# Kernel tuning notes

Measured on AMD Instinct MI355X. Metric: run time of the kernel, lower is better.

## Reference

```python
import jax, jax.numpy as jnp
import numpy as np
from jax import lax

B = 128

# ---- 4-qubit statevector helpers (RY + CNOT circuit is real-valued) ----

def _init_state(n):
    s = jnp.zeros((n, 2, 2, 2, 2), jnp.float32)
    return s.at[:, 0, 0, 0, 0].set(1.0)


def _ry(state, theta, wire):
    # RY(t) = [[cos t/2, -sin t/2],[sin t/2, cos t/2]]; theta: scalar or [N]
    s = jnp.moveaxis(state, wire + 1, 1)
    c = jnp.cos(theta * 0.5)
    sn = jnp.sin(theta * 0.5)
    if jnp.ndim(theta) > 0:
        c = c.reshape(-1, 1, 1, 1)
        sn = sn.reshape(-1, 1, 1, 1)
    a, b = s[:, 0], s[:, 1]
    s = jnp.stack([c * a - sn * b, sn * a + c * b], axis=1)
    return jnp.moveaxis(s, 1, wire + 1)


def _cnot(state, ctrl, tgt):
    s = jnp.moveaxis(state, [ctrl + 1, tgt + 1], [1, 2])
    s = jnp.concatenate([s[:, :1], jnp.flip(s[:, 1:], axis=2)], axis=1)
    return jnp.moveaxis(s, [1, 2], [ctrl + 1, tgt + 1])


def _random_layer(state, thetas):
    for i in range(4):
        state = _ry(state, thetas[i], i)
        state = _cnot(state, i, (i + 1) % 4)
    return state


def _measure_z(state, wire):
    p = jnp.moveaxis(state, wire + 1, 1) ** 2
    p = p.reshape(p.shape[0], 2, -1).sum(-1)
    return p[:, 0] - p[:, 1]


def setup_inputs() -> dict:
    key = jax.random.key(0)
    ks = jax.random.split(key, 12)

    def n(k, shape, scale):
        return jax.random.normal(k, shape, jnp.float32) * scale

    return {
        "x": jax.random.normal(ks[0], (B, 3, 249, 249), jnp.float32),
        "conv1_w": n(ks[1], (6, 3, 5, 5), 0.1),
        "conv1_b": jnp.zeros((6,), jnp.float32),
        "conv2_w": n(ks[2], (15, 6, 3, 3), 0.1),
        "conv2_b": jnp.zeros((15,), jnp.float32),
        "fc1_w": n(ks[3], (120, 55815), 1.0 / np.sqrt(55815.0)),
        "fc1_b": jnp.zeros((120,), jnp.float32),
        "fc2_w": n(ks[4], (84, 120), 1.0 / np.sqrt(120.0)),
        "fc2_b": jnp.zeros((84,), jnp.float32),
        "fc3_w": n(ks[5], (1, 84), 1.0 / np.sqrt(84.0)),
        "fc3_b": jnp.zeros((1,), jnp.float32),
        "head_thetas": jax.random.uniform(ks[6], (4,), jnp.float32, 0.0, 2.0 * np.pi),
        "qf_thetas": jax.random.uniform(ks[7], (4,), jnp.float32, 0.0, 2.0 * np.pi),
        "lin_w": n(ks[8], (1, 784), 1.0 / np.sqrt(784.0)),
        "lin_b": jnp.zeros((1,), jnp.float32),
    }


def reference(x, conv1_w, conv1_b, conv2_w, conv2_b, fc1_w, fc1_b, fc2_w, fc2_b,
              fc3_w, fc3_b, head_thetas, qf_thetas, lin_w, lin_b):
    bsz = x.shape[0]

    def conv(y, w, b, stride):
        y = lax.conv_general_dilated(y, w, (stride, stride), [(1, 1), (1, 1)],
                                     dimension_numbers=("NCHW", "OIHW", "NCHW"))
        return y + b[None, :, None, None]

    def pool(y):  # MaxPool2d(kernel=2, stride=1)
        return lax.reduce_window(y, -jnp.inf, lax.max, (1, 1, 2, 2), (1, 1, 1, 1), "VALID")

    # ---- conv branch (dropout = identity in eval) ----
    h = pool(jax.nn.relu(conv(x, conv1_w, conv1_b, 2)))          # [B,6,123,123]
    h = pool(jax.nn.relu(conv(h, conv2_w, conv2_b, 2)))          # [B,15,61,61]
    h = h.reshape(bsz, -1)                                        # [B,55815]
    h = jax.nn.relu(h @ fc1_w.T + fc1_b)
    h = jax.nn.relu(h @ fc2_w.T + fc2_b)
    logit = (h @ fc3_w.T + fc3_b)[:, 0]                           # [B]
    st = _init_state(bsz)
    st = _ry(st, logit, 0)
    st = _random_layer(st, head_thetas)
    probs_conv = jax.nn.sigmoid(_measure_z(st, 0))[:, None]       # [B,1]

    # ---- quanvolution branch ----
    gray = x.mean(axis=1, keepdims=True)                          # [B,1,249,249]
    g = jax.image.resize(gray, (bsz, 1, 28, 28), method="linear")[:, 0]
    # 2x2 patches, row-major, element order [tl, tr, bl, br]
    patches = g.reshape(bsz, 14, 2, 14, 2).transpose(0, 1, 3, 2, 4).reshape(bsz * 196, 4)
    st = _init_state(bsz * 196)
    for w in range(4):
        st = _ry(st, patches[:, w], w)
    st = _random_layer(st, qf_thetas)
    feats = jnp.stack([_measure_z(st, w) for w in range(4)], axis=1).reshape(bsz, 784)
    probs_q = jax.nn.sigmoid(feats @ lin_w.T + lin_b)             # [B,1]

    probs = (probs_conv + probs_q) * 0.5
    return jnp.concatenate([probs, 1.0 - probs], axis=-1)         # [B,2]
```

## Files before the change

kernel.cpp:

```cpp
#include <hip/hip_runtime.h>
#include <math.h>

#define DEV static __device__ __forceinline__

template <int W>
DEV void q_ry(float s[16], float th) {
  float c = cosf(th * 0.5f), sn = sinf(th * 0.5f);
  constexpr int m = 8 >> W;
#pragma unroll
  for (int i = 0; i < 16; ++i) {
    if (!(i & m)) {
      float a = s[i], b = s[i | m];
      s[i] = c * a - sn * b;
      s[i | m] = sn * a + c * b;
    }
  }
}
template <int C, int T>
DEV void q_cnot(float s[16]) {
  constexpr int mc = 8 >> C, mt = 8 >> T;
#pragma unroll
  for (int i = 0; i < 16; ++i) {
    if ((i & mc) && !(i & mt)) {
      float t = s[i]; s[i] = s[i | mt]; s[i | mt] = t;
    }
  }
}
template <int W>
DEV float q_mz(const float s[16]) {
  constexpr int m = 8 >> W;
  float p = 0.f;
#pragma unroll
  for (int i = 0; i < 16; ++i) p += (i & m) ? -s[i] * s[i] : s[i] * s[i];
  return p;
}
DEV void q_layer(float s[16], const float* __restrict__ th) {
  q_ry<0>(s, th[0]); q_cnot<0, 1>(s);
  q_ry<1>(s, th[1]); q_cnot<1, 2>(s);
  q_ry<2>(s, th[2]); q_cnot<2, 3>(s);
  q_ry<3>(s, th[3]); q_cnot<3, 0>(s);
}

__global__ __launch_bounds__(256, 4) void k_conv1(const float* __restrict__ x,
                                                  const float* __restrict__ w,
                                                  const float* __restrict__ bia,
                                                  float* __restrict__ out) {
  __shared__ float smem[3 * 87 * 38];
  float (*xs)[87][38] = (float (*)[87][38])smem;
  float (*ct)[42][19] = (float (*)[42][19])smem;
  int b = blockIdx.z;
  int PY0 = blockIdx.y * 41, PX0 = blockIdx.x * 16;
  int iy0 = PY0 * 2 - 1, ix0 = PX0 * 2 - 1;
  int tid = threadIdx.x;
  const float* xb = x + (size_t)b * 186003;
  for (int idx = tid; idx < 3 * 87 * 38; idx += 256) {
    int ci = idx / 3306, rem = idx % 3306, rr = rem / 38, cc = rem % 38;
    int iy = iy0 + rr, ix = ix0 + cc;
    float v = 0.f;
    if (cc < 37 && iy >= 0 && iy < 249 && ix >= 0 && ix < 249)
      v = xb[ci * 62001 + iy * 249 + ix];
    xs[ci][rr][cc] = v;
  }
  __syncthreads();
  int co = tid % 6, r = tid / 6;
  float acc[17];
  if (tid < 252) {
    float bv = bia[co];
#pragma unroll
    for (int t = 0; t < 17; ++t) acc[t] = bv;
    for (int ci = 0; ci < 3; ++ci) {
      float wreg[25];
#pragma unroll
      for (int j = 0; j < 25; ++j) wreg[j] = w[co * 75 + ci * 25 + j];
#pragma unroll
      for (int ky = 0; ky < 5; ++ky) {
        const float* xrow = &xs[ci][2 * r + ky][0];
        float xv[38];
#pragma unroll
        for (int j = 0; j < 19; ++j) {
          float2 t2 = *reinterpret_cast<const float2*>(&xrow[2 * j]);
          xv[2 * j] = t2.x; xv[2 * j + 1] = t2.y;
        }
#pragma unroll
        for (int tx = 0; tx < 17; ++tx)
#pragma unroll
          for (int kx = 0; kx < 5; ++kx)
            acc[tx] += xv[2 * tx + kx] * wreg[ky * 5 + kx];
      }
    }
  }
  __syncthreads();
  if (tid < 252) {
#pragma unroll
    for (int tx = 0; tx < 17; ++tx) ct[co][r][tx] = acc[tx];
  }
  __syncthreads();
  for (int i = tid; i < 6 * 41 * 16; i += 256) {
    int co2 = i / 656, rem = i % 656, pr = rem / 16, pc = rem % 16;
    int py = PY0 + pr, px = PX0 + pc;
    if (px < 123) {
      float m = fmaxf(fmaxf(ct[co2][pr][pc], ct[co2][pr][pc + 1]),
                      fmaxf(ct[co2][pr + 1][pc], ct[co2][pr + 1][pc + 1]));
      out[((size_t)(b * 6 + co2) * 123 + py) * 123 + px] = fmaxf(m, 0.f);
    }
  }
}

__global__ __launch_bounds__(256, 4) void k_conv2(const float* __restrict__ in,
                                                  const float* __restrict__ w,
                                                  const float* __restrict__ bia,
                                                  float* __restrict__ out) {
  __shared__ float smem[6 * 35 * 36];
  float (*xs)[35][36] = (float (*)[35][36])smem;
  float (*ct)[17][18] = (float (*)[17][18])smem;
  int b = blockIdx.z;
  int py0 = blockIdx.y * 16, px0 = blockIdx.x * 16;
  int iy0 = py0 * 2 - 1, ix0 = px0 * 2 - 1;
  int tid = threadIdx.x;
  const float* ib = in + (size_t)b * 90774;
  for (int idx = tid; idx < 6 * 35 * 36; idx += 256) {
    int ci = idx / 1260, rem = idx % 1260, rr = rem / 36, cc = rem % 36;
    int iy = iy0 + rr, ix = ix0 + cc;
    float v = 0.f;
    if (cc < 35 && iy >= 0 && iy < 123 && ix >= 0 && ix < 123)
      v = ib[ci * 15129 + iy * 123 + ix];
    xs[ci][rr][cc] = v;
  }
  __syncthreads();
  int co = tid % 15, ty = tid / 15;
  float acc[17];
  if (tid < 255) {
    float bv = bia[co];
#pragma unroll
    for (int t = 0; t < 17; ++t) acc[t] = bv;
#pragma unroll
    for (int ci = 0; ci < 6; ++ci) {
      float wreg[9];
#pragma unroll
      for (int j = 0; j < 9; ++j) wreg[j] = w[co * 54 + ci * 9 + j];
#pragma unroll
      for (int ky = 0; ky < 3; ++ky) {
        const float* xrow = &xs[ci][2 * ty + ky][0];
        float xv[36];
#pragma unroll
        for (int j = 0; j < 18; ++j) {
          float2 t2 = *reinterpret_cast<const float2*>(&xrow[2 * j]);
          xv[2 * j] = t2.x; xv[2 * j + 1] = t2.y;
        }
#pragma unroll
        for (int tx = 0; tx < 17; ++tx)
#pragma unroll
          for (int kx = 0; kx < 3; ++kx)
            acc[tx] += xv[2 * tx + kx] * wreg[ky * 3 + kx];
      }
    }
  }
  __syncthreads();
  if (tid < 255) {
#pragma unroll
    for (int tx = 0; tx < 17; ++tx) ct[co][ty][tx] = acc[tx];
  }
  __syncthreads();
  for (int i = tid; i < 15 * 16 * 16; i += 256) {
    int co2 = i / 256, rem = i % 256, pr = rem / 16, pc = rem % 16;
    int py = py0 + pr, px = px0 + pc;
    if (py < 61 && px < 61) {
      float m = fmaxf(fmaxf(ct[co2][pr][pc], ct[co2][pr][pc + 1]),
                      fmaxf(ct[co2][pr + 1][pc], ct[co2][pr + 1][pc + 1]));
      out[(size_t)b * 55815 + co2 * 3721 + py * 61 + px] = fmaxf(m, 0.f);
    }
  }
}

#define KFC 55815
#define NCHUNK 1745
#define FC1_BLOCKS 512
__global__ __launch_bounds__(256) void k_fc1(const float* __restrict__ h,
                                             const float* __restrict__ w,
                                             float* __restrict__ partial) {
  __shared__ float hs[128][33];
  __shared__ float wsd[120][33];
  int tid = threadIdx.x;
  int tb = tid & 31;
  int bo = tid >> 5;
  float acc[4][15];
#pragma unroll
  for (int j = 0; j < 4; ++j)
#pragma unroll
    for (int oo = 0; oo < 15; ++oo) acc[j][oo] = 0.f;

  for (int ch = blockIdx.x; ch < NCHUNK; ch += FC1_BLOCKS) {
    int k0 = ch * 32;
    for (int idx = tid; idx < 128 * 32; idx += 256) {
      int bb = idx >> 5, kk = idx & 31;
      int k = k0 + kk;
      hs[bb][kk] = (k < KFC) ? h[(size_t)bb * KFC + k] : 0.f;
    }
    for (int idx = tid; idx < 120 * 32; idx += 256) {
      int oo = idx >> 5, kk = idx & 31;
      int k = k0 + kk;
      wsd[oo][kk] = (k < KFC) ? w[(size_t)oo * KFC + k] : 0.f;
    }
    __syncthreads();
#pragma unroll 4
    for (int kk = 0; kk < 32; ++kk) {
      float hv[4], wv[15];
#pragma unroll
      for (int j = 0; j < 4; ++j) hv[j] = hs[tb + 32 * j][kk];
#pragma unroll
      for (int oo = 0; oo < 15; ++oo) wv[oo] = wsd[bo * 15 + oo][kk];
#pragma unroll
      for (int j = 0; j < 4; ++j)
#pragma unroll
        for (int oo = 0; oo < 15; ++oo) acc[j][oo] += hv[j] * wv[oo];
    }
    __syncthreads();
  }
  float* pg = partial + (size_t)blockIdx.x * 15360;
#pragma unroll
  for (int j = 0; j < 4; ++j) {
    int b = tb + 32 * j;
#pragma unroll
    for (int oo = 0; oo < 15; ++oo) pg[b * 120 + bo * 15 + oo] = acc[j][oo];
  }
}

__global__ __launch_bounds__(256) void k_fc1_reduce(const float* __restrict__ partial,
                                                    const float* __restrict__ bias,
                                                    float* __restrict__ outv) {
  int i = blockIdx.x * 256 + threadIdx.x;
  if (i >= 15360) return;
  float a = bias[i % 120];
  for (int g = 0; g < FC1_BLOCKS; ++g) a += partial[(size_t)g * 15360 + i];
  outv[i] = fmaxf(a, 0.f);
}

__global__ __launch_bounds__(128) void k_head(const float* __restrict__ fc1o,
                                              const float* __restrict__ w2,
                                              const float* __restrict__ b2,
                                              const float* __restrict__ w3,
                                              const float* __restrict__ b3,
                                              const float* __restrict__ hth,
                                              float* __restrict__ probs_conv) {
  __shared__ float h1[120];
  __shared__ float h2[84];
  int b = blockIdx.x, tid = threadIdx.x;
  if (tid < 120) h1[tid] = fc1o[b * 120 + tid];
  __syncthreads();
  if (tid < 84) {
    float a = b2[tid];
    for (int k = 0; k < 120; ++k) a += h1[k] * w2[tid * 120 + k];
    h2[tid] = fmaxf(a, 0.f);
  }
  __syncthreads();
  if (tid == 0) {
    float lg = b3[0];
    for (int j = 0; j < 84; ++j) lg += h2[j] * w3[j];
    float s[16];
#pragma unroll
    for (int i = 0; i < 16; ++i) s[i] = 0.f;
    s[0] = 1.f;
    q_ry<0>(s, lg);
    q_layer(s, hth);
    float z = q_mz<0>(s);
    probs_conv[b] = 1.f / (1.f + expf(-z));
  }
}

DEV void resize_win(int o, int& i0, int& i1, float& sf, float& inorm) {
  const float invs = 249.0f / 28.0f;
  sf = ((float)o + 0.5f) * invs - 0.5f;
  i0 = (int)ceilf(sf - invs); if (i0 < 0) i0 = 0;
  i1 = (int)floorf(sf + invs); if (i1 > 248) i1 = 248;
  float nrm = 0.f;
  for (int i = i0; i <= i1; ++i)
    nrm += fmaxf(0.f, 1.f - fabsf(sf - (float)i) * (28.0f / 249.0f));
  inorm = 1.f / nrm;
}

__global__ __launch_bounds__(256) void k_resize_rows(const float* __restrict__ x,
                                                     float* __restrict__ tmp) {
  int b = blockIdx.x / 28, oy = blockIdx.x % 28;
  int ix = threadIdx.x;
  if (ix >= 249) return;
  int i0, i1; float sf, inorm;
  resize_win(oy, i0, i1, sf, inorm);
  const float* xb = x + (size_t)b * 186003;
  float acc = 0.f;
  for (int iy = i0; iy <= i1; ++iy) {
    float wv = fmaxf(0.f, 1.f - fabsf(sf - (float)iy) * (28.0f / 249.0f)) * inorm;
    float gr = (xb[iy * 249 + ix] + xb[62001 + iy * 249 + ix] +
                xb[124002 + iy * 249 + ix]) * (1.0f / 3.0f);
    acc += wv * gr;
  }
  tmp[((size_t)b * 28 + oy) * 249 + ix] = acc;
}

__global__ __launch_bounds__(256) void k_quanv(const float* __restrict__ tmp,
                                               const float* __restrict__ qth,
                                               const float* __restrict__ lw,
                                               const float* __restrict__ lb,
                                               const float* __restrict__ probs_conv,
                                               float* __restrict__ out) {
  __shared__ float g[784];
  __shared__ float red[4];
  int b = blockIdx.x, tid = threadIdx.x;
  for (int idx = tid; idx < 784; idx += 256) {
    int oy = idx / 28, ox = idx % 28;
    int i0, i1; float sf, inorm;
    resize_win(ox, i0, i1, sf, inorm);
    const float* tr = tmp + ((size_t)b * 28 + oy) * 249;
    float acc = 0.f;
    for (int i = i0; i <= i1; ++i)
      acc += fmaxf(0.f, 1.f - fabsf(sf - (float)i) * (28.0f / 249.0f)) * inorm * tr[i];
    g[idx] = acc;
  }
  __syncthreads();
  float part = 0.f;
  if (tid < 196) {
    int pi = tid / 14, pj = tid % 14;
    float v0 = g[(2 * pi) * 28 + 2 * pj];
    float v1 = g[(2 * pi) * 28 + 2 * pj + 1];
    float v2 = g[(2 * pi + 1) * 28 + 2 * pj];
    float v3 = g[(2 * pi + 1) * 28 + 2 * pj + 1];
    float s[16];
#pragma unroll
    for (int i = 0; i < 16; ++i) s[i] = 0.f;
    s[0] = 1.f;
    q_ry<0>(s, v0); q_ry<1>(s, v1); q_ry<2>(s, v2); q_ry<3>(s, v3);
    q_layer(s, qth);
    float z0 = q_mz<0>(s), z1 = q_mz<1>(s), z2 = q_mz<2>(s), z3 = q_mz<3>(s);
    const float* lwp = lw + tid * 4;
    part = z0 * lwp[0] + z1 * lwp[1] + z2 * lwp[2] + z3 * lwp[3];
  }
#pragma unroll
  for (int off = 32; off > 0; off >>= 1) part += __shfl_down(part, off, 64);
  if ((tid & 63) == 0) red[tid >> 6] = part;
  __syncthreads();
  if (tid == 0) {
    float tot = red[0] + red[1] + red[2] + red[3] + lb[0];
    float pq = 1.f / (1.f + expf(-tot));
    float pr = 0.5f * (probs_conv[b] + pq);
    out[b * 2 + 0] = pr;
    out[b * 2 + 1] = 1.f - pr;
  }
}

extern "C" void kernel_launch(void* const* d_in, const int* in_sizes, int n_in,
                              void* d_out, int out_size, void* d_ws, size_t ws_size,
                              hipStream_t stream) {
  const float* x   = (const float*)d_in[0];
  const float* c1w = (const float*)d_in[1];
  const float* c1b = (const float*)d_in[2];
  const float* c2w = (const float*)d_in[3];
  const float* c2b = (const float*)d_in[4];
  const float* f1w = (const float*)d_in[5];
  const float* f1b = (const float*)d_in[6];
  const float* f2w = (const float*)d_in[7];
  const float* f2b = (const float*)d_in[8];
  const float* f3w = (const float*)d_in[9];
  const float* f3b = (const float*)d_in[10];
  const float* hth = (const float*)d_in[11];
  const float* qth = (const float*)d_in[12];
  const float* lw  = (const float*)d_in[13];
  const float* lb  = (const float*)d_in[14];
  float* out = (float*)d_out;
  char* ws = (char*)d_ws;

  float* pool1   = (float*)(ws);
  float* partial = pool1;
  float* h       = (float*)(ws + 46476288);
  float* tmp     = (float*)(ws + 75053568);
  float* fc1o    = (float*)(ws + 78623232);
  float* pconv   = (float*)(ws + 78684672);

  k_conv1<<<dim3(8, 3, 128), 256, 0, stream>>>(x, c1w, c1b, pool1);
  k_conv2<<<dim3(4, 4, 128), 256, 0, stream>>>(pool1, c2w, c2b, h);
  k_fc1<<<dim3(FC1_BLOCKS), 256, 0, stream>>>(h, f1w, partial);
  k_fc1_reduce<<<dim3(60), 256, 0, stream>>>(partial, f1b, fc1o);
  k_head<<<dim3(128), 128, 0, stream>>>(fc1o, f2w, f2b, f3w, f3b, hth, pconv);
  k_resize_rows<<<dim3(128 * 28), 256, 0, stream>>>(x, tmp);
  k_quanv<<<dim3(128), 256, 0, stream>>>(tmp, qth, lw, lb, pconv, out);
}
```

Baseline: 283.0 us.

## Restructure conv1/conv2 so each thread computes all output channels over column segments

The conv kernels change their thread mapping. Before, each thread handled one output channel across a full row of 17 columns. Now each thread computes every output channel for a small column segment, so each loaded input value is reused across channels. A new small pre-kernel reorders the conv weights so each (ci,ky) slice loads as a contiguous block. conv2 also uses taller tiles (31 rows) and stages input channels in two phases to fit shared memory, which halves the block count in y. The risks are extra register pressure from the larger accumulator and weight arrays, uneven work for the thread that handles the last column in conv2, and one extra kernel launch.

```diff
diff --git a/kernel.cpp b/kernel.cpp
--- a/kernel.cpp
+++ b/kernel.cpp
@@ -41,133 +41,190 @@
   q_ry<3>(s, th[3]); q_cnot<3, 0>(s);
 }
 
+__global__ void k_wre(const float* __restrict__ c1w, const float* __restrict__ c2w,
+                      float* __restrict__ wre1, float* __restrict__ wre2) {
+  int t = blockIdx.x * 256 + threadIdx.x;
+  if (t < 450) {
+    int g = t / 30, rem = t % 30;
+    int ci = g / 5, ky = g % 5, kx = rem / 6, co = rem % 6;
+    wre1[t] = c1w[co * 75 + ci * 25 + ky * 5 + kx];
+  }
+  if (t < 810) {
+    int g = t / 45, rem = t % 45;
+    int ci = g / 3, ky = g % 3, kx = rem / 15, co = rem % 15;
+    wre2[t] = c2w[co * 54 + ci * 9 + ky * 3 + kx];
+  }
+}
+
 __global__ __launch_bounds__(256, 4) void k_conv1(const float* __restrict__ x,
-                                                  const float* __restrict__ w,
+                                                  const float* __restrict__ wre1,
                                                   const float* __restrict__ bia,
                                                   float* __restrict__ out) {
-  __shared__ float smem[3 * 87 * 38];
-  float (*xs)[87][38] = (float (*)[87][38])smem;
+  __shared__ float smem[9920];
   float (*ct)[42][19] = (float (*)[42][19])smem;
   int b = blockIdx.z;
   int PY0 = blockIdx.y * 41, PX0 = blockIdx.x * 16;
   int iy0 = PY0 * 2 - 1, ix0 = PX0 * 2 - 1;
   int tid = threadIdx.x;
   const float* xb = x + (size_t)b * 186003;
-  for (int idx = tid; idx < 3 * 87 * 38; idx += 256) {
-    int ci = idx / 3306, rem = idx % 3306, rr = rem / 38, cc = rem % 38;
+#pragma unroll
+  for (int s = 0; s < 39; ++s) {
+    int idx = s * 256 + tid;
+    bool ok = idx < 9918;
+    int ci = idx / 3306, rem = idx - ci * 3306;
+    int rr = rem / 38, cc = rem - rr * 38;
     int iy = iy0 + rr, ix = ix0 + cc;
     float v = 0.f;
-    if (cc < 37 && iy >= 0 && iy < 249 && ix >= 0 && ix < 249)
+    if (ok && cc < 37 && (unsigned)iy < 249u && (unsigned)ix < 249u)
       v = xb[ci * 62001 + iy * 249 + ix];
-    xs[ci][rr][cc] = v;
-  }
-  __syncthreads();
-  int co = tid % 6, r = tid / 6;
-  float acc[17];
+    if (ok) smem[idx] = v;
+  }
+  __syncthreads();
+  int r = tid / 6, seg = tid - 6 * (tid / 6);
+  float acc[6][3];
   if (tid < 252) {
-    float bv = bia[co];
-#pragma unroll
-    for (int t = 0; t < 17; ++t) acc[t] = bv;
-    for (int ci = 0; ci < 3; ++ci) {
-      float wreg[25];
-#pragma unroll
-      for (int j = 0; j < 25; ++j) wreg[j] = w[co * 75 + ci * 25 + j];
+#pragma unroll
+    for (int co = 0; co < 6; ++co) {
+      float bv = bia[co];
+#pragma unroll
+      for (int c = 0; c < 3; ++c) acc[co][c] = bv;
+    }
+#pragma unroll
+    for (int ci = 0; ci < 3; ++ci)
 #pragma unroll
       for (int ky = 0; ky < 5; ++ky) {
-        const float* xrow = &xs[ci][2 * r + ky][0];
-        float xv[38];
-#pragma unroll
-        for (int j = 0; j < 19; ++j) {
+        const float* xrow = &smem[(ci * 87 + 2 * r + ky) * 38 + 6 * seg];
+        float xv[10];
+#pragma unroll
+        for (int j = 0; j < 5; ++j) {
           float2 t2 = *reinterpret_cast<const float2*>(&xrow[2 * j]);
           xv[2 * j] = t2.x; xv[2 * j + 1] = t2.y;
         }
-#pragma unroll
-        for (int tx = 0; tx < 17; ++tx)
+        const float* wp = wre1 + (ci * 5 + ky) * 30;
+        float wr[30];
+#pragma unroll
+        for (int j = 0; j < 30; ++j) wr[j] = wp[j];
+#pragma unroll
+        for (int c = 0; c < 3; ++c)
 #pragma unroll
           for (int kx = 0; kx < 5; ++kx)
-            acc[tx] += xv[2 * tx + kx] * wreg[ky * 5 + kx];
+#pragma unroll
+            for (int co = 0; co < 6; ++co)
+              acc[co][c] += xv[2 * c + kx] * wr[kx * 6 + co];
       }
-    }
   }
   __syncthreads();
   if (tid < 252) {
 #pragma unroll
-    for (int tx = 0; tx < 17; ++tx) ct[co][r][tx] = acc[tx];
-  }
-  __syncthreads();
-  for (int i = tid; i < 6 * 41 * 16; i += 256) {
-    int co2 = i / 656, rem = i % 656, pr = rem / 16, pc = rem % 16;
-    int py = PY0 + pr, px = PX0 + pc;
-    if (px < 123) {
-      float m = fmaxf(fmaxf(ct[co2][pr][pc], ct[co2][pr][pc + 1]),
-                      fmaxf(ct[co2][pr + 1][pc], ct[co2][pr + 1][pc + 1]));
-      out[((size_t)(b * 6 + co2) * 123 + py) * 123 + px] = fmaxf(m, 0.f);
+    for (int co = 0; co < 6; ++co)
+#pragma unroll
+      for (int c = 0; c < 3; ++c)
+        if (3 * seg + c < 17) ct[co][r][3 * seg + c] = acc[co][c];
+  }
+  __syncthreads();
+#pragma unroll
+  for (int co2 = 0; co2 < 6; ++co2) {
+    for (int j = tid; j < 41 * 16; j += 256) {
+      int pr = j >> 4, pc = j & 15;
+      int px = PX0 + pc;
+      if (px < 123) {
+        float m = fmaxf(fmaxf(ct[co2][pr][pc], ct[co2][pr][pc + 1]),
+                        fmaxf(ct[co2][pr + 1][pc], ct[co2][pr + 1][pc + 1]));
+        out[((size_t)(b * 6 + co2) * 123 + PY0 + pr) * 123 + px] = fmaxf(m, 0.f);
+      }
     }
   }
 }
 
 __global__ __launch_bounds__(256, 4) void k_conv2(const float* __restrict__ in,
-                                                  const float* __restrict__ w,
+                                                  const float* __restrict__ wre2,
                                                   const float* __restrict__ bia,
                                                   float* __restrict__ out) {
-  __shared__ float smem[6 * 35 * 36];
-  float (*xs)[35][36] = (float (*)[35][36])smem;
-  float (*ct)[17][18] = (float (*)[17][18])smem;
+  __shared__ float smem[8160];
+  float (*ct)[32][17] = (float (*)[32][17])smem;
   int b = blockIdx.z;
-  int py0 = blockIdx.y * 16, px0 = blockIdx.x * 16;
-  int iy0 = py0 * 2 - 1, ix0 = px0 * 2 - 1;
+  int ty_tile = blockIdx.y;
+  int CY0 = ty_tile * 31;
+  int CX0 = blockIdx.x * 16;
+  int IY0 = 2 * CY0 - 1, IX0 = 2 * CX0 - 1;
   int tid = threadIdx.x;
+  int r = tid >> 3, seg = tid & 7;
   const float* ib = in + (size_t)b * 90774;
-  for (int idx = tid; idx < 6 * 35 * 36; idx += 256) {
-    int ci = idx / 1260, rem = idx % 1260, rr = rem / 36, cc = rem % 36;
-    int iy = iy0 + rr, ix = ix0 + cc;
-    float v = 0.f;
-    if (cc < 35 && iy >= 0 && iy < 123 && ix >= 0 && ix < 123)
-      v = ib[ci * 15129 + iy * 123 + ix];
-    xs[ci][rr][cc] = v;
-  }
-  __syncthreads();
-  int co = tid % 15, ty = tid / 15;
-  float acc[17];
-  if (tid < 255) {
+  float acc[15][3];
+#pragma unroll
+  for (int co = 0; co < 15; ++co) {
     float bv = bia[co];
 #pragma unroll
-    for (int t = 0; t < 17; ++t) acc[t] = bv;
-#pragma unroll
-    for (int ci = 0; ci < 6; ++ci) {
-      float wreg[9];
-#pragma unroll
-      for (int j = 0; j < 9; ++j) wreg[j] = w[co * 54 + ci * 9 + j];
+    for (int c = 0; c < 3; ++c) acc[co][c] = bv;
+  }
+#pragma unroll
+  for (int phase = 0; phase < 2; ++phase) {
+    if (phase) __syncthreads();
+#pragma unroll
+    for (int s = 0; s < 28; ++s) {
+      int idx = s * 256 + tid;
+      bool ok = idx < 7020;
+      int cil = idx / 2340, rem = idx - cil * 2340;
+      int rr = rem / 36, cc = rem - rr * 36;
+      int iy = IY0 + rr, ix = IX0 + cc;
+      float v = 0.f;
+      if (ok && cc < 35 && (unsigned)iy < 123u && (unsigned)ix < 123u)
+        v = ib[(3 * phase + cil) * 15129 + iy * 123 + ix];
+      if (ok) smem[idx] = v;
+    }
+    __syncthreads();
+#pragma unroll
+    for (int cil = 0; cil < 3; ++cil)
 #pragma unroll
       for (int ky = 0; ky < 3; ++ky) {
-        const float* xrow = &xs[ci][2 * ty + ky][0];
-        float xv[36];
-#pragma unroll
-        for (int j = 0; j < 18; ++j) {
+        const float* xrow = &smem[(cil * 65 + 2 * r + ky) * 36 + 4 * seg];
+        float xv[8];
+#pragma unroll
+        for (int j = 0; j < 4; ++j) {
           float2 t2 = *reinterpret_cast<const float2*>(&xrow[2 * j]);
           xv[2 * j] = t2.x; xv[2 * j + 1] = t2.y;
         }
-#pragma unroll
-        for (int tx = 0; tx < 17; ++tx)
+        const float* wp = wre2 + ((3 * phase + cil) * 3 + ky) * 45;
+        float wr[45];
+#pragma unroll
+        for (int j = 0; j < 45; ++j) wr[j] = wp[j];
+#pragma unroll
+        for (int c = 0; c < 2; ++c)
 #pragma unroll
           for (int kx = 0; kx < 3; ++kx)
-            acc[tx] += xv[2 * tx + kx] * wreg[ky * 3 + kx];
+#pragma unroll
+            for (int co = 0; co < 15; ++co)
+              acc[co][c] += xv[2 * c + kx] * wr[kx * 15 + co];
+        if (seg == 7) {
+#pragma unroll
+          for (int kx = 0; kx < 3; ++kx)
+#pragma unroll
+            for (int co = 0; co < 15; ++co)
+              acc[co][2] += xv[4 + kx] * wr[kx * 15 + co];
+        }
       }
-    }
-  }
-  __syncthreads();
-  if (tid < 255) {
-#pragma unroll
-    for (int tx = 0; tx < 17; ++tx) ct[co][ty][tx] = acc[tx];
-  }
-  __syncthreads();
-  for (int i = tid; i < 15 * 16 * 16; i += 256) {
-    int co2 = i / 256, rem = i % 256, pr = rem / 16, pc = rem % 16;
-    int py = py0 + pr, px = px0 + pc;
-    if (py < 61 && px < 61) {
-      float m = fmaxf(fmaxf(ct[co2][pr][pc], ct[co2][pr][pc + 1]),
-                      fmaxf(ct[co2][pr + 1][pc], ct[co2][pr + 1][pc + 1]));
-      out[(size_t)b * 55815 + co2 * 3721 + py * 61 + px] = fmaxf(m, 0.f);
+  }
+  __syncthreads();
+  if (CY0 + r < 62) {
+#pragma unroll
+    for (int co = 0; co < 15; ++co) {
+      ct[co][r][2 * seg] = acc[co][0];
+      ct[co][r][2 * seg + 1] = acc[co][1];
+      if (seg == 7) ct[co][r][16] = acc[co][2];
+    }
+  }
+  __syncthreads();
+  int PRN = (ty_tile == 0) ? 31 : 30;
+#pragma unroll
+  for (int co2 = 0; co2 < 15; ++co2) {
+    for (int j = tid; j < PRN * 16; j += 256) {
+      int pr = j >> 4, pc = j & 15;
+      int py = CY0 + pr, px = CX0 + pc;
+      if (px < 61) {
+        float m = fmaxf(fmaxf(ct[co2][pr][pc], ct[co2][pr][pc + 1]),
+                        fmaxf(ct[co2][pr + 1][pc], ct[co2][pr + 1][pc + 1]));
+        out[(size_t)b * 55815 + co2 * 3721 + py * 61 + px] = fmaxf(m, 0.f);
+      }
     }
   }
 }
@@ -373,9 +430,12 @@
   float* tmp     = (float*)(ws + 75053568);
   float* fc1o    = (float*)(ws + 78623232);
   float* pconv   = (float*)(ws + 78684672);
-
-  k_conv1<<<dim3(8, 3, 128), 256, 0, stream>>>(x, c1w, c1b, pool1);
-  k_conv2<<<dim3(4, 4, 128), 256, 0, stream>>>(pool1, c2w, c2b, h);
+  float* wre1    = (float*)(ws + 78685184);
+  float* wre2    = (float*)(ws + 78686984);
+
+  k_wre<<<dim3(4), 256, 0, stream>>>(c1w, c2w, wre1, wre2);
+  k_conv1<<<dim3(8, 3, 128), 256, 0, stream>>>(x, wre1, c1b, pool1);
+  k_conv2<<<dim3(4, 2, 128), 256, 0, stream>>>(pool1, wre2, c2b, h);
   k_fc1<<<dim3(FC1_BLOCKS), 256, 0, stream>>>(h, f1w, partial);
   k_fc1_reduce<<<dim3(60), 256, 0, stream>>>(partial, f1b, fc1o);
   k_head<<<dim3(128), 128, 0, stream>>>(fc1o, f2w, f2b, f3w, f3b, hth, pconv);
```

New measurement: 429.3 us. 1.52x slower.

## Restructure conv1 thread mapping to compute all output channels per thread segment

Applied to the files above, without the earlier changes.

conv1 now assigns each thread a row and a 3-column segment and accumulates all six output channels, with weights pre-transposed by a small k_wre kernel so each weight load feeds six channels and the per-thread input window shrinks. The smem staging loop is fully unrolled with unsigned bounds checks. The pool1 output row stride is padded to 128, and conv2 reads with the padded stride. The quanvolution kernel is split into two half-image blocks per batch item, with a tiny final kernel combining the partial sums, which adds two extra launches.

```diff
diff --git a/kernel.cpp b/kernel.cpp
--- a/kernel.cpp
+++ b/kernel.cpp
@@ -41,67 +41,88 @@
   q_ry<3>(s, th[3]); q_cnot<3, 0>(s);
 }
 
+__global__ void k_wre(const float* __restrict__ c1w, float* __restrict__ wre1) {
+  int t = blockIdx.x * 256 + threadIdx.x;
+  if (t < 450) {
+    int g = t / 30, rem = t % 30;
+    int ci = g / 5, ky = g % 5, kx = rem / 6, co = rem % 6;
+    wre1[t] = c1w[co * 75 + ci * 25 + ky * 5 + kx];
+  }
+}
+
 __global__ __launch_bounds__(256, 4) void k_conv1(const float* __restrict__ x,
-                                                  const float* __restrict__ w,
+                                                  const float* __restrict__ wre1,
                                                   const float* __restrict__ bia,
                                                   float* __restrict__ out) {
-  __shared__ float smem[3 * 87 * 38];
-  float (*xs)[87][38] = (float (*)[87][38])smem;
+  __shared__ float smem[9920];
   float (*ct)[42][19] = (float (*)[42][19])smem;
   int b = blockIdx.z;
   int PY0 = blockIdx.y * 41, PX0 = blockIdx.x * 16;
   int iy0 = PY0 * 2 - 1, ix0 = PX0 * 2 - 1;
   int tid = threadIdx.x;
   const float* xb = x + (size_t)b * 186003;
-  for (int idx = tid; idx < 3 * 87 * 38; idx += 256) {
-    int ci = idx / 3306, rem = idx % 3306, rr = rem / 38, cc = rem % 38;
+#pragma unroll
+  for (int s = 0; s < 39; ++s) {
+    int idx = s * 256 + tid;
+    bool ok = idx < 9918;
+    int ci = idx / 3306, rem = idx - ci * 3306;
+    int rr = rem / 38, cc = rem - rr * 38;
     int iy = iy0 + rr, ix = ix0 + cc;
     float v = 0.f;
-    if (cc < 37 && iy >= 0 && iy < 249 && ix >= 0 && ix < 249)
+    if (ok && cc < 37 && (unsigned)iy < 249u && (unsigned)ix < 249u)
       v = xb[ci * 62001 + iy * 249 + ix];
-    xs[ci][rr][cc] = v;
-  }
-  __syncthreads();
-  int co = tid % 6, r = tid / 6;
-  float acc[17];
+    if (ok) smem[idx] = v;
+  }
+  __syncthreads();
+  int r = tid / 6, seg = tid - 6 * (tid / 6);
+  float acc[6][3];
   if (tid < 252) {
-    float bv = bia[co];
-#pragma unroll
-    for (int t = 0; t < 17; ++t) acc[t] = bv;
-    for (int ci = 0; ci < 3; ++ci) {
-      float wreg[25];
-#pragma unroll
-      for (int j = 0; j < 25; ++j) wreg[j] = w[co * 75 + ci * 25 + j];
+#pragma unroll
+    for (int co = 0; co < 6; ++co) {
+      float bv = bia[co];
+#pragma unroll
+      for (int c = 0; c < 3; ++c) acc[co][c] = bv;
+    }
+#pragma unroll
+    for (int ci = 0; ci < 3; ++ci)
 #pragma unroll
       for (int ky = 0; ky < 5; ++ky) {
-        const float* xrow = &xs[ci][2 * r + ky][0];
-        float xv[38];
-#pragma unroll
-        for (int j = 0; j < 19; ++j) {
+        const float* xrow = &smem[(ci * 87 + 2 * r + ky) * 38 + 6 * seg];
+        float xv[10];
+#pragma unroll
+        for (int j = 0; j < 5; ++j) {
           float2 t2 = *reinterpret_cast<const float2*>(&xrow[2 * j]);
           xv[2 * j] = t2.x; xv[2 * j + 1] = t2.y;
         }
-#pragma unroll
-        for (int tx = 0; tx < 17; ++tx)
+        const float* wp = wre1 + (ci * 5 + ky) * 30;
+        float wr[30];
+#pragma unroll
+        for (int j = 0; j < 30; ++j) wr[j] = wp[j];
+#pragma unroll
+        for (int c = 0; c < 3; ++c)
 #pragma unroll
           for (int kx = 0; kx < 5; ++kx)
-            acc[tx] += xv[2 * tx + kx] * wreg[ky * 5 + kx];
+#pragma unroll
+            for (int co = 0; co < 6; ++co)
+              acc[co][c] += xv[2 * c + kx] * wr[kx * 6 + co];
       }
-    }
   }
   __syncthreads();
   if (tid < 252) {
 #pragma unroll
-    for (int tx = 0; tx < 17; ++tx) ct[co][r][tx] = acc[tx];
-  }
-  __syncthreads();
-  for (int i = tid; i < 6 * 41 * 16; i += 256) {
-    int co2 = i / 656, rem = i % 656, pr = rem / 16, pc = rem % 16;
-    int py = PY0 + pr, px = PX0 + pc;
-    if (px < 123) {
+    for (int co = 0; co < 6; ++co)
+#pragma unroll
+      for (int c = 0; c < 3; ++c)
+        if (3 * seg + c < 17) ct[co][r][3 * seg + c] = acc[co][c];
+  }
+  __syncthreads();
+#pragma unroll
+  for (int co2 = 0; co2 < 6; ++co2) {
+    for (int j = tid; j < 41 * 16; j += 256) {
+      int pr = j >> 4, pc = j & 15;
       float m = fmaxf(fmaxf(ct[co2][pr][pc], ct[co2][pr][pc + 1]),
                       fmaxf(ct[co2][pr + 1][pc], ct[co2][pr + 1][pc + 1]));
-      out[((size_t)(b * 6 + co2) * 123 + py) * 123 + px] = fmaxf(m, 0.f);
+      out[((size_t)(b * 6 + co2) * 123 + PY0 + pr) * 128 + PX0 + pc] = fmaxf(m, 0.f);
     }
   }
 }
@@ -117,13 +138,13 @@
   int py0 = blockIdx.y * 16, px0 = blockIdx.x * 16;
   int iy0 = py0 * 2 - 1, ix0 = px0 * 2 - 1;
   int tid = threadIdx.x;
-  const float* ib = in + (size_t)b * 90774;
+  const float* ib = in + (size_t)b * 94464;
   for (int idx = tid; idx < 6 * 35 * 36; idx += 256) {
     int ci = idx / 1260, rem = idx % 1260, rr = rem / 36, cc = rem % 36;
     int iy = iy0 + rr, ix = ix0 + cc;
     float v = 0.f;
-    if (cc < 35 && iy >= 0 && iy < 123 && ix >= 0 && ix < 123)
-      v = ib[ci * 15129 + iy * 123 + ix];
+    if (cc < 35 && (unsigned)iy < 123u && (unsigned)ix < 123u)
+      v = ib[ci * 15744 + iy * 128 + ix];
     xs[ci][rr][cc] = v;
   }
   __syncthreads();
@@ -299,14 +320,15 @@
 __global__ __launch_bounds__(256) void k_quanv(const float* __restrict__ tmp,
                                                const float* __restrict__ qth,
                                                const float* __restrict__ lw,
-                                               const float* __restrict__ lb,
-                                               const float* __restrict__ probs_conv,
-                                               float* __restrict__ out) {
-  __shared__ float g[784];
+                                               float* __restrict__ qpart) {
+  __shared__ float g[392];
   __shared__ float red[4];
-  int b = blockIdx.x, tid = threadIdx.x;
-  for (int idx = tid; idx < 784; idx += 256) {
-    int oy = idx / 28, ox = idx % 28;
+  int bid = blockIdx.x;
+  int b = bid >> 1, half = bid & 1;
+  int tid = threadIdx.x;
+  for (int idx = tid; idx < 392; idx += 256) {
+    int ly = idx / 28, ox = idx % 28;
+    int oy = 14 * half + ly;
     int i0, i1; float sf, inorm;
     resize_win(ox, i0, i1, sf, inorm);
     const float* tr = tmp + ((size_t)b * 28 + oy) * 249;
@@ -317,12 +339,13 @@
   }
   __syncthreads();
   float part = 0.f;
-  if (tid < 196) {
-    int pi = tid / 14, pj = tid % 14;
-    float v0 = g[(2 * pi) * 28 + 2 * pj];
-    float v1 = g[(2 * pi) * 28 + 2 * pj + 1];
-    float v2 = g[(2 * pi + 1) * 28 + 2 * pj];
-    float v3 = g[(2 * pi + 1) * 28 + 2 * pj + 1];
+  if (tid < 98) {
+    int pl = tid / 14, pj = tid % 14;
+    int pi = 7 * half + pl;
+    float v0 = g[(2 * pl) * 28 + 2 * pj];
+    float v1 = g[(2 * pl) * 28 + 2 * pj + 1];
+    float v2 = g[(2 * pl + 1) * 28 + 2 * pj];
+    float v3 = g[(2 * pl + 1) * 28 + 2 * pj + 1];
     float s[16];
 #pragma unroll
     for (int i = 0; i < 16; ++i) s[i] = 0.f;
@@ -330,20 +353,26 @@
     q_ry<0>(s, v0); q_ry<1>(s, v1); q_ry<2>(s, v2); q_ry<3>(s, v3);
     q_layer(s, qth);
     float z0 = q_mz<0>(s), z1 = q_mz<1>(s), z2 = q_mz<2>(s), z3 = q_mz<3>(s);
-    const float* lwp = lw + tid * 4;
+    const float* lwp = lw + (pi * 14 + pj) * 4;
     part = z0 * lwp[0] + z1 * lwp[1] + z2 * lwp[2] + z3 * lwp[3];
   }
 #pragma unroll
   for (int off = 32; off > 0; off >>= 1) part += __shfl_down(part, off, 64);
   if ((tid & 63) == 0) red[tid >> 6] = part;
   __syncthreads();
-  if (tid == 0) {
-    float tot = red[0] + red[1] + red[2] + red[3] + lb[0];
-    float pq = 1.f / (1.f + expf(-tot));
-    float pr = 0.5f * (probs_conv[b] + pq);
-    out[b * 2 + 0] = pr;
-    out[b * 2 + 1] = 1.f - pr;
-  }
+  if (tid == 0) qpart[bid] = red[0] + red[1] + red[2] + red[3];
+}
+
+__global__ __launch_bounds__(128) void k_final(const float* __restrict__ qpart,
+                                               const float* __restrict__ lb,
+                                               const float* __restrict__ probs_conv,
+                                               float* __restrict__ out) {
+  int b = threadIdx.x;
+  float tot = qpart[2 * b] + qpart[2 * b + 1] + lb[0];
+  float pq = 1.f / (1.f + expf(-tot));
+  float pr = 0.5f * (probs_conv[b] + pq);
+  out[b * 2 + 0] = pr;
+  out[b * 2 + 1] = 1.f - pr;
 }
 
 extern "C" void kernel_launch(void* const* d_in, const int* in_sizes, int n_in,
@@ -368,17 +397,21 @@
   char* ws = (char*)d_ws;
 
   float* pool1   = (float*)(ws);
-  float* partial = pool1;
-  float* h       = (float*)(ws + 46476288);
-  float* tmp     = (float*)(ws + 75053568);
-  float* fc1o    = (float*)(ws + 78623232);
-  float* pconv   = (float*)(ws + 78684672);
-
-  k_conv1<<<dim3(8, 3, 128), 256, 0, stream>>>(x, c1w, c1b, pool1);
+  float* partial = (float*)(ws);
+  float* tmp     = (float*)(ws + 33554432);
+  float* h       = (float*)(ws + 48365568);
+  float* fc1o    = (float*)(ws + 76942848);
+  float* pconv   = (float*)(ws + 77004288);
+  float* wre1    = (float*)(ws + 77004800);
+  float* qpart   = (float*)(ws + 77009848);
+
+  k_wre<<<dim3(2), 256, 0, stream>>>(c1w, wre1);
+  k_conv1<<<dim3(8, 3, 128), 256, 0, stream>>>(x, wre1, c1b, pool1);
   k_conv2<<<dim3(4, 4, 128), 256, 0, stream>>>(pool1, c2w, c2b, h);
   k_fc1<<<dim3(FC1_BLOCKS), 256, 0, stream>>>(h, f1w, partial);
   k_fc1_reduce<<<dim3(60), 256, 0, stream>>>(partial, f1b, fc1o);
   k_head<<<dim3(128), 128, 0, stream>>>(fc1o, f2w, f2b, f3w, f3b, hth, pconv);
   k_resize_rows<<<dim3(128 * 28), 256, 0, stream>>>(x, tmp);
-  k_quanv<<<dim3(128), 256, 0, stream>>>(tmp, qth, lw, lb, pconv, out);
-}
+  k_quanv<<<dim3(256), 256, 0, stream>>>(tmp, qth, lw, qpart);
+  k_final<<<dim3(1), 128, 0, stream>>>(qpart, lb, pconv, out);
+}
```

Result: faster. 265.9 us (-6.1%).
